# Performance work log

Hardware: AMD Instinct MI355X
Metric: run time of the kernel (lower is better)

The kernel has to match this reference:

```python
import jax, jax.numpy as jnp
import numpy as np

B, IN, OUT = 256, 1024, 1024

def leaky_clamp(x, lo, hi, slope):
    return jnp.where(x < lo, lo + slope * (x - lo),
           jnp.where(x > hi, hi + slope * (x - hi), x))

def setup_inputs() -> dict:
    key = jax.random.key(0)
    kx, kw = jax.random.split(key)
    x = jax.random.normal(kx, (B, IN), dtype=jnp.float32)
    # xavier_normal for (out,in): std = sqrt(2/(in+out))
    std = np.sqrt(2.0 / (IN + OUT)).astype(np.float32)
    weight = jax.random.normal(kw, (OUT, IN), dtype=jnp.float32) * std
    log_tau = jnp.zeros((), dtype=jnp.float32)
    return {"x": x, "weight": weight, "log_tau": log_tau}

def reference(x, weight, log_tau):
    # actual_weight = leaky_clamp(weight, 0, 1, 0.1)
    aw = leaky_clamp(weight, 0.0, 1.0, 0.1)          # (OUT, IN)
    tau = jnp.exp(log_tau)                            # scalar
    z = x[:, None, :] * aw[None, :, :]                # (B, OUT, IN)
    p = jax.nn.softmax(tau * z, axis=-1)              # (B, OUT, IN)
    s = jnp.sum(p * z, axis=-1)                       # (B, OUT)
    return s
```

## Files before the change

kernel.cpp:

```cpp
#include <hip/hip_runtime.h>

#define BB   256
#define IN_  1024
#define OUTN 1024

#define TB  32
#define TO  16
#define KC  256
#define PAD 4

#define LOG2E 1.4426950408889634f

__device__ __forceinline__ float leaky_clamp01(float v) {
    float lo  = fminf(v, 0.0f);
    float hi  = fmaxf(v - 1.0f, 0.0f);
    float mid = fminf(fmaxf(v, 0.0f), 1.0f);
    return fmaf(0.1f, lo + hi, mid);
}

__global__ __launch_bounds__(256, 2)
void esm_fused_kernel(const float* __restrict__ x,
                      const float* __restrict__ w,
                      const float* __restrict__ log_tau,
                      float* __restrict__ out) {
    __shared__ float xs[TB][KC + PAD];
    __shared__ float wls[TO][KC + PAD];

    const int tid = threadIdx.x;
    const int bid = blockIdx.x;
    const int bt = bid >> 6;
    const int ot = bid & 63;
    const int b0 = bt * TB;
    const int o0 = ot * TO;

    const float scale = __expf(log_tau[0]) * LOG2E;

    const int tx  = tid & 15;
    const int ty  = tid >> 4;
    const int r0  = 2 * ty;

    float d0 = 0.f, d1 = 0.f, n0 = 0.f, n1 = 0.f;

    for (int s = 0; s < IN_ / KC; ++s) {
        const int i0 = s * KC;
        __syncthreads();
        #pragma unroll
        for (int t = 0; t < 8; ++t) {
            const int f   = tid + t * 256;
            const int row = f >> 6;
            const int i4  = (f & 63) << 2;
            const float4 v = *(const float4*)&x[(size_t)(b0 + row) * IN_ + i0 + i4];
            float4 xv;
            xv.x = v.x * scale; xv.y = v.y * scale;
            xv.z = v.z * scale; xv.w = v.w * scale;
            *(float4*)&xs[row][i4] = xv;
        }
        #pragma unroll
        for (int t = 0; t < 4; ++t) {
            const int f   = tid + t * 256;
            const int row = f >> 6;
            const int i4  = (f & 63) << 2;
            const float4 v = *(const float4*)&w[(size_t)(o0 + row) * IN_ + i0 + i4];
            float4 wv;
            wv.x = leaky_clamp01(v.x); wv.y = leaky_clamp01(v.y);
            wv.z = leaky_clamp01(v.z); wv.w = leaky_clamp01(v.w);
            *(float4*)&wls[row][i4] = wv;
        }
        __syncthreads();

        #pragma unroll 4
        for (int i = 0; i < KC; i += 4) {
            const float4 xa = *(const float4*)&xs[r0][i];
            const float4 xb = *(const float4*)&xs[r0 + 1][i];
            const float4 wa = *(const float4*)&wls[tx][i];

            #define ACC1(xe, we, dd, nn) { float t_ = (xe) * (we); \
                float e_ = __builtin_amdgcn_exp2f(t_); dd += e_; nn = fmaf(e_, t_, nn); }
            ACC1(xa.x, wa.x, d0, n0) ACC1(xa.y, wa.y, d0, n0)
            ACC1(xa.z, wa.z, d0, n0) ACC1(xa.w, wa.w, d0, n0)
            ACC1(xb.x, wa.x, d1, n1) ACC1(xb.y, wa.y, d1, n1)
            ACC1(xb.z, wa.z, d1, n1) ACC1(xb.w, wa.w, d1, n1)
            #undef ACC1
        }
    }

    const size_t base = (size_t)(b0 + r0) * OUTN + o0 + tx;
    out[base]        = n0 / (d0 * scale);
    out[base + OUTN] = n1 / (d1 * scale);
}

extern "C" void kernel_launch(void* const* d_in, const int* in_sizes, int n_in,
                              void* d_out, int out_size, void* d_ws, size_t ws_size,
                              hipStream_t stream) {
    const float* x  = (const float*)d_in[0];
    const float* w  = (const float*)d_in[1];
    const float* lt = (const float*)d_in[2];
    float* out = (float*)d_out;

    esm_fused_kernel<<<(BB / TB) * (OUTN / TO), 256, 0, stream>>>(x, w, lt, out);
}
```

Before: 101.5 us.

## Halve batch tile to one output per thread with split accumulators

Cuts the batch tile from 32 to 16 rows, so each thread computes a single output instead of two. The kernel now launches twice as many blocks and requests four blocks per SM instead of two. The x and weight staging loops are merged into one, and the inner loop splits the exp-sum and weighted-sum into two independent accumulator pairs to give the exp2 chain more instruction-level parallelism. In exchange, each x value is reused only once per weight load instead of twice. That raises shared-memory reads per exponential and doubles global re-reads of the weight tile.

```diff
diff --git a/kernel.cpp b/kernel.cpp
--- a/kernel.cpp
+++ b/kernel.cpp
@@ -4,7 +4,7 @@
 #define IN_  1024
 #define OUTN 1024
 
-#define TB  32
+#define TB  16
 #define TO  16
 #define KC  256
 #define PAD 4
@@ -18,7 +18,7 @@
     return fmaf(0.1f, lo + hi, mid);
 }
 
-__global__ __launch_bounds__(256, 2)
+__global__ __launch_bounds__(256, 4)
 void esm_fused_kernel(const float* __restrict__ x,
                       const float* __restrict__ w,
                       const float* __restrict__ log_tau,
@@ -35,17 +35,16 @@
 
     const float scale = __expf(log_tau[0]) * LOG2E;
 
-    const int tx  = tid & 15;
-    const int ty  = tid >> 4;
-    const int r0  = 2 * ty;
+    const int tx = tid & 15;
+    const int ty = tid >> 4;
 
-    float d0 = 0.f, d1 = 0.f, n0 = 0.f, n1 = 0.f;
+    float da = 0.f, db = 0.f, na = 0.f, nb = 0.f;
 
     for (int s = 0; s < IN_ / KC; ++s) {
         const int i0 = s * KC;
         __syncthreads();
         #pragma unroll
-        for (int t = 0; t < 8; ++t) {
+        for (int t = 0; t < 4; ++t) {
             const int f   = tid + t * 256;
             const int row = f >> 6;
             const int i4  = (f & 63) << 2;
@@ -54,39 +53,34 @@
             xv.x = v.x * scale; xv.y = v.y * scale;
             xv.z = v.z * scale; xv.w = v.w * scale;
             *(float4*)&xs[row][i4] = xv;
-        }
-        #pragma unroll
-        for (int t = 0; t < 4; ++t) {
-            const int f   = tid + t * 256;
-            const int row = f >> 6;
-            const int i4  = (f & 63) << 2;
-            const float4 v = *(const float4*)&w[(size_t)(o0 + row) * IN_ + i0 + i4];
+            const float4 u = *(const float4*)&w[(size_t)(o0 + row) * IN_ + i0 + i4];
             float4 wv;
-            wv.x = leaky_clamp01(v.x); wv.y = leaky_clamp01(v.y);
-            wv.z = leaky_clamp01(v.z); wv.w = leaky_clamp01(v.w);
+            wv.x = leaky_clamp01(u.x); wv.y = leaky_clamp01(u.y);
+            wv.z = leaky_clamp01(u.z); wv.w = leaky_clamp01(u.w);
             *(float4*)&wls[row][i4] = wv;
         }
         __syncthreads();
 
         #pragma unroll 4
         for (int i = 0; i < KC; i += 4) {
-            const float4 xa = *(const float4*)&xs[r0][i];
-            const float4 xb = *(const float4*)&xs[r0 + 1][i];
+            const float4 xa = *(const float4*)&xs[ty][i];
             const float4 wa = *(const float4*)&wls[tx][i];
-
-            #define ACC1(xe, we, dd, nn) { float t_ = (xe) * (we); \
-                float e_ = __builtin_amdgcn_exp2f(t_); dd += e_; nn = fmaf(e_, t_, nn); }
-            ACC1(xa.x, wa.x, d0, n0) ACC1(xa.y, wa.y, d0, n0)
-            ACC1(xa.z, wa.z, d0, n0) ACC1(xa.w, wa.w, d0, n0)
-            ACC1(xb.x, wa.x, d1, n1) ACC1(xb.y, wa.y, d1, n1)
-            ACC1(xb.z, wa.z, d1, n1) ACC1(xb.w, wa.w, d1, n1)
-            #undef ACC1
+            const float t0 = xa.x * wa.x;
+            const float t1 = xa.y * wa.y;
+            const float t2 = xa.z * wa.z;
+            const float t3 = xa.w * wa.w;
+            const float e0 = __builtin_amdgcn_exp2f(t0);
+            const float e1 = __builtin_amdgcn_exp2f(t1);
+            const float e2 = __builtin_amdgcn_exp2f(t2);
+            const float e3 = __builtin_amdgcn_exp2f(t3);
+            da += e0; db += e1;
+            na = fmaf(e0, t0, na); nb = fmaf(e1, t1, nb);
+            da += e2; db += e3;
+            na = fmaf(e2, t2, na); nb = fmaf(e3, t3, nb);
         }
     }
 
-    const size_t base = (size_t)(b0 + r0) * OUTN + o0 + tx;
-    out[base]        = n0 / (d0 * scale);
-    out[base + OUTN] = n1 / (d1 * scale);
+    out[(size_t)(b0 + ty) * OUTN + o0 + tx] = (na + nb) / ((da + db) * scale);
 }
 
 extern "C" void kernel_launch(void* const* d_in, const int* in_sizes, int n_in,
```

Result: faster. 94.27 us (-7.1%).

## Restructure tiling to stream x from global and prefetch weights via registers

Applied to the files above, without the earlier changes.

Retiles each block to 8 batch rows by 64 outputs, keeping only the clamped, tau-scaled weights in LDS. Each wavefront reads its two x rows directly from global memory as wave-uniform broadcasts. Weight chunks are prefetched into registers one stage ahead to overlap global loads with exp work. It also rewrites leaky clamp as a single med3, splits the accumulators to shorten dependency chains, and uses a raw waitcnt+barrier. The costs are more global x traffic, reliance on cache for the broadcast loads, and higher register pressure from the prefetch buffer.

```diff
diff --git a/kernel.cpp b/kernel.cpp
--- a/kernel.cpp
+++ b/kernel.cpp
@@ -4,18 +4,20 @@
 #define IN_  1024
 #define OUTN 1024
 
-#define TB  32
-#define TO  16
-#define KC  256
-#define PAD 4
+#define TB   8
+#define TO   64
+#define KC   128
+#define NSTG (IN_ / KC)
+#define PAD  4
 
 #define LOG2E 1.4426950408889634f
 
+__device__ __forceinline__ void lds_barrier() {
+    asm volatile("s_waitcnt lgkmcnt(0)\n\ts_barrier" ::: "memory");
+}
+
 __device__ __forceinline__ float leaky_clamp01(float v) {
-    float lo  = fminf(v, 0.0f);
-    float hi  = fmaxf(v - 1.0f, 0.0f);
-    float mid = fminf(fmaxf(v, 0.0f), 1.0f);
-    return fmaf(0.1f, lo + hi, mid);
+    return __builtin_amdgcn_fmed3f(v, 0.1f * v, fmaf(0.1f, v, 0.9f));
 }
 
 __global__ __launch_bounds__(256, 2)
@@ -23,70 +25,87 @@
                       const float* __restrict__ w,
                       const float* __restrict__ log_tau,
                       float* __restrict__ out) {
-    __shared__ float xs[TB][KC + PAD];
     __shared__ float wls[TO][KC + PAD];
 
     const int tid = threadIdx.x;
     const int bid = blockIdx.x;
-    const int bt = bid >> 6;
-    const int ot = bid & 63;
+    const int ot = bid & 15;
+    const int bt = bid >> 4;
     const int b0 = bt * TB;
     const int o0 = ot * TO;
 
     const float scale = __expf(log_tau[0]) * LOG2E;
 
-    const int tx  = tid & 15;
-    const int ty  = tid >> 4;
-    const int r0  = 2 * ty;
+    const int lane = tid & 63;
+    const int wv   = __builtin_amdgcn_readfirstlane(tid >> 6);
+    const float* xr0 = x + (size_t)(b0 + 2 * wv) * IN_;
+    const float* xr1 = xr0 + IN_;
 
-    float d0 = 0.f, d1 = 0.f, n0 = 0.f, n1 = 0.f;
+    const int srow = tid >> 5;
+    const int si4  = (tid & 31) << 2;
 
-    for (int s = 0; s < IN_ / KC; ++s) {
-        const int i0 = s * KC;
-        __syncthreads();
+    float4 rw[8];
+    #pragma unroll
+    for (int t = 0; t < 8; ++t)
+        rw[t] = *(const float4*)&w[(size_t)(o0 + srow + 8 * t) * IN_ + si4];
+
+    float d0a = 0.f, d0b = 0.f, n0a = 0.f, n0b = 0.f;
+    float d1a = 0.f, d1b = 0.f, n1a = 0.f, n1b = 0.f;
+
+    #pragma unroll
+    for (int s = 0; s < NSTG; ++s) {
+        if (s) lds_barrier();
         #pragma unroll
         for (int t = 0; t < 8; ++t) {
-            const int f   = tid + t * 256;
-            const int row = f >> 6;
-            const int i4  = (f & 63) << 2;
-            const float4 v = *(const float4*)&x[(size_t)(b0 + row) * IN_ + i0 + i4];
-            float4 xv;
-            xv.x = v.x * scale; xv.y = v.y * scale;
-            xv.z = v.z * scale; xv.w = v.w * scale;
-            *(float4*)&xs[row][i4] = xv;
+            const float4 v = rw[t];
+            float4 o4;
+            o4.x = leaky_clamp01(v.x) * scale;
+            o4.y = leaky_clamp01(v.y) * scale;
+            o4.z = leaky_clamp01(v.z) * scale;
+            o4.w = leaky_clamp01(v.w) * scale;
+            *(float4*)&wls[srow + 8 * t][si4] = o4;
         }
-        #pragma unroll
-        for (int t = 0; t < 4; ++t) {
-            const int f   = tid + t * 256;
-            const int row = f >> 6;
-            const int i4  = (f & 63) << 2;
-            const float4 v = *(const float4*)&w[(size_t)(o0 + row) * IN_ + i0 + i4];
-            float4 wv;
-            wv.x = leaky_clamp01(v.x); wv.y = leaky_clamp01(v.y);
-            wv.z = leaky_clamp01(v.z); wv.w = leaky_clamp01(v.w);
-            *(float4*)&wls[row][i4] = wv;
+        if (s + 1 < NSTG) {
+            const int gbase = (s + 1) * KC;
+            #pragma unroll
+            for (int t = 0; t < 8; ++t)
+                rw[t] = *(const float4*)&w[(size_t)(o0 + srow + 8 * t) * IN_ + gbase + si4];
         }
-        __syncthreads();
+        lds_barrier();
 
+        const int gi0 = s * KC;
         #pragma unroll 4
         for (int i = 0; i < KC; i += 4) {
-            const float4 xa = *(const float4*)&xs[r0][i];
-            const float4 xb = *(const float4*)&xs[r0 + 1][i];
-            const float4 wa = *(const float4*)&wls[tx][i];
+            const float4 w4 = *(const float4*)&wls[lane][i];
+            const float4 x0 = *(const float4*)(xr0 + gi0 + i);
+            const float4 x1 = *(const float4*)(xr1 + gi0 + i);
 
-            #define ACC1(xe, we, dd, nn) { float t_ = (xe) * (we); \
-                float e_ = __builtin_amdgcn_exp2f(t_); dd += e_; nn = fmaf(e_, t_, nn); }
-            ACC1(xa.x, wa.x, d0, n0) ACC1(xa.y, wa.y, d0, n0)
-            ACC1(xa.z, wa.z, d0, n0) ACC1(xa.w, wa.w, d0, n0)
-            ACC1(xb.x, wa.x, d1, n1) ACC1(xb.y, wa.y, d1, n1)
-            ACC1(xb.z, wa.z, d1, n1) ACC1(xb.w, wa.w, d1, n1)
-            #undef ACC1
+            const float t00 = x0.x * w4.x, t01 = x0.y * w4.y;
+            const float t02 = x0.z * w4.z, t03 = x0.w * w4.w;
+            const float t10 = x1.x * w4.x, t11 = x1.y * w4.y;
+            const float t12 = x1.z * w4.z, t13 = x1.w * w4.w;
+
+            const float e00 = __builtin_amdgcn_exp2f(t00);
+            const float e01 = __builtin_amdgcn_exp2f(t01);
+            const float e02 = __builtin_amdgcn_exp2f(t02);
+            const float e03 = __builtin_amdgcn_exp2f(t03);
+            const float e10 = __builtin_amdgcn_exp2f(t10);
+            const float e11 = __builtin_amdgcn_exp2f(t11);
+            const float e12 = __builtin_amdgcn_exp2f(t12);
+            const float e13 = __builtin_amdgcn_exp2f(t13);
+
+            d0a += e00; d0b += e01; d0a += e02; d0b += e03;
+            n0a = fmaf(e00, t00, n0a); n0b = fmaf(e01, t01, n0b);
+            n0a = fmaf(e02, t02, n0a); n0b = fmaf(e03, t03, n0b);
+            d1a += e10; d1b += e11; d1a += e12; d1b += e13;
+            n1a = fmaf(e10, t10, n1a); n1b = fmaf(e11, t11, n1b);
+            n1a = fmaf(e12, t12, n1a); n1b = fmaf(e13, t13, n1b);
         }
     }
 
-    const size_t base = (size_t)(b0 + r0) * OUTN + o0 + tx;
-    out[base]        = n0 / (d0 * scale);
-    out[base + OUTN] = n1 / (d1 * scale);
+    const size_t base = (size_t)(b0 + 2 * wv) * OUTN + o0 + lane;
+    out[base]        = (n0a + n0b) / ((d0a + d0b) * scale);
+    out[base + OUTN] = (n1a + n1b) / ((d1a + d1b) * scale);
 }
 
 extern "C" void kernel_launch(void* const* d_in, const int* in_sizes, int n_in,
```

Measured after the change: 102.8 us. No clear change (+1.3%).
